# Optimization experiments

Measured on AMD Instinct MI355X. Metric: run time of the kernel, lower is better.

The kernel has to match this reference:

```python
import jax, jax.numpy as jnp
import numpy as np

B, S, H, M = 8, 128, 768, 128
EPS = 1e-12


def setup_inputs() -> dict:
    key = jax.random.key(0)
    ks = jax.random.split(key, 8)
    seq_hiddens = jax.random.normal(ks[0], (B, S, H), dtype=jnp.float32)
    gamma = jnp.ones((H,), jnp.float32)
    beta = jnp.zeros((H,), jnp.float32)
    # conditional LN dense weights (torch Linear weight: (out, in)); small init so math stays stable
    w_beta = jax.random.normal(ks[1], (H, H), dtype=jnp.float32) * 0.02
    w_gamma = jax.random.normal(ks[2], (H, H), dtype=jnp.float32) * 0.02
    w_ent = jax.random.normal(ks[3], (H, M), dtype=jnp.float32) * 0.02
    w_head = jax.random.normal(ks[4], (H, M), dtype=jnp.float32) * 0.02
    w_tail = jax.random.normal(ks[5], (H, M), dtype=jnp.float32) * 0.02
    b_ent = jnp.zeros((M,), jnp.float32)
    b_head = jnp.zeros((M,), jnp.float32)
    b_tail = jnp.zeros((M,), jnp.float32)
    return dict(seq_hiddens=seq_hiddens, gamma=gamma, beta=beta, w_beta=w_beta,
                w_gamma=w_gamma, w_ent=w_ent, b_ent=b_ent, w_head=w_head,
                b_head=b_head, w_tail=w_tail, b_tail=b_tail)


def _handshake_cln(seq, gamma, beta, w_beta, w_gamma):
    # Triangular pair expansion in the same row-major order as the torch loop:
    # for ind in range(S): pairs (ind, ind), (ind, ind+1), ..., (ind, S-1)
    s = seq.shape[1]
    ii, jj = jnp.triu_indices(s)                 # (P,) each, P = S(S+1)/2
    x = seq[:, jj, :]                            # visible hiddens   (B, P, H)
    cond = seq[:, ii, :]                         # repeated hiddens  (B, P, H)
    beta_c = jnp.einsum('bph,oh->bpo', cond, w_beta) + beta      # (B, P, H)
    gamma_c = jnp.einsum('bph,oh->bpo', cond, w_gamma) + gamma   # (B, P, H)
    mean = jnp.mean(x, axis=-1, keepdims=True)
    out = x - mean
    var = jnp.mean(out * out, axis=-1, keepdims=True)
    std = (var + EPS) ** 2                       # NOTE: faithful to source (no sqrt)
    return out / std * gamma_c + beta_c


def reference(seq_hiddens, gamma, beta, w_beta, w_gamma, w_ent, b_ent,
              w_head, b_head, w_tail, b_tail):
    shaking = _handshake_cln(seq_hiddens, gamma, beta, w_beta, w_gamma)  # (B, P, H)
    ent = jnp.tanh(shaking @ w_ent + b_ent)      # (B, P, M)
    head = jnp.tanh(shaking @ w_head + b_head)
    tail = jnp.tanh(shaking @ w_tail + b_tail)
    return jnp.stack([ent, head, tail], axis=0)  # (3, B, P, M)
```

## Files before the change

kernel.cpp:

```cpp
#include <hip/hip_runtime.h>
#include <hip/hip_bf16.h>
#include <hip/hip_fp16.h>
#include <math.h>

#define B_   8
#define S_   128
#define H_   768
#define M_   128
#define P_   8256
#define BP_  66048
#define EPSF 1e-12f

typedef unsigned short u16;
typedef unsigned int   u32;
typedef _Float16 h16;
typedef _Float16 ffrag __attribute__((ext_vector_type(8)));
typedef float    f32x16 __attribute__((ext_vector_type(16)));

__device__ __forceinline__ u32 fuse2(u32 x, u32 g, u32 b) {
    __half2 r = __hfma2(__builtin_bit_cast(__half2, x),
                        __builtin_bit_cast(__half2, g),
                        __builtin_bit_cast(__half2, b));
    return __builtin_bit_cast(u32, r);
}
__device__ __forceinline__ float fast_tanh(float v) {
    float t = __expf(v + v);
    float r = __builtin_amdgcn_rcpf(t + 1.0f);
    return fmaf(-2.0f, r, 1.0f);
}
__device__ __forceinline__ void gl_lds16(const h16* g, h16* l) {
    __builtin_amdgcn_global_load_lds(
        (const __attribute__((address_space(1))) u32*)g,
        (__attribute__((address_space(3))) u32*)l, 16, 0, 0);
}
__device__ __forceinline__ uint4 cvt8(float4 a, float4 b) {
    h16 v[8];
    v[0] = (h16)a.x; v[1] = (h16)a.y; v[2] = (h16)a.z; v[3] = (h16)a.w;
    v[4] = (h16)b.x; v[5] = (h16)b.y; v[6] = (h16)b.z; v[7] = (h16)b.w;
    return *reinterpret_cast<uint4*>(v);
}

#define CONDB 768
#define WPK0  768
#define BIAS0 792
#define NORM0 794
__global__ __launch_bounds__(256) void k_pre(
    const float* __restrict__ seq,
    const float* __restrict__ wg, const float* __restrict__ wb,
    const float* __restrict__ we, const float* __restrict__ wh,
    const float* __restrict__ wt,
    const float* __restrict__ gamma, const float* __restrict__ beta,
    const float* __restrict__ be, const float* __restrict__ bh,
    const float* __restrict__ bt,
    h16* __restrict__ wpk, float* __restrict__ biasc,
    h16* __restrict__ xn, h16* __restrict__ Gc, h16* __restrict__ Bc)
{
    __shared__ __align__(16) char smem[24576];
    const int bx = blockIdx.x;
    const int t = threadIdx.x;

    if (bx < CONDB) {
        h16* Ash = (h16*)smem;
        h16* Bsh = (h16*)smem + 64 * 72;
        const int rbx = bx & 15, by = bx >> 4;
        const int row0 = rbx * 64;
        const bool isg = (by < 24);
        const int nc0 = (isg ? by : by - 24) * 32;
        const float* wsrc = isg ? wg : wb;

        const int r = t >> 2, q = t & 3;
        const float* ap = seq + (size_t)(row0 + r) * H_ + q * 16;
        h16* asto = &Ash[r * 72 + q * 16];
        const int rb = t >> 3, qb = t & 7;
        const float* wp = wsrc + (size_t)(nc0 + rb) * H_ + qb * 8;
        h16* bsto = &Bsh[rb * 72 + qb * 8];

        const int lane = t & 63, wid = t >> 6;
        const int wm0 = (wid >> 1) * 32, wn0 = (wid & 1) * 16;
        const int l15 = lane & 15, quad = lane >> 4, q8 = quad * 8;

        typedef float f32x4 __attribute__((ext_vector_type(4)));
        f32x4 acc[2] = {};
        for (int kt = 0; kt < 12; ++kt) {
            const int k0 = kt * 64;
            float4 a0 = *(const float4*)(ap + k0);      float4 a1 = *(const float4*)(ap + k0 + 4);
            float4 a2 = *(const float4*)(ap + k0 + 8);  float4 a3 = *(const float4*)(ap + k0 + 12);
            float4 w0 = *(const float4*)(wp + k0);      float4 w1 = *(const float4*)(wp + k0 + 4);
            *(uint4*)asto = cvt8(a0, a1); *(uint4*)(asto + 8) = cvt8(a2, a3);
            *(uint4*)bsto = cvt8(w0, w1);
            __syncthreads();
#pragma unroll
            for (int ks = 0; ks < 64; ks += 32) {
                ffrag af[2], bf;
#pragma unroll
                for (int mi = 0; mi < 2; ++mi)
                    af[mi] = *reinterpret_cast<const ffrag*>(&Ash[(wm0 + mi * 16 + l15) * 72 + ks + q8]);
                bf = *reinterpret_cast<const ffrag*>(&Bsh[(wn0 + l15) * 72 + ks + q8]);
#pragma unroll
                for (int mi = 0; mi < 2; ++mi)
                    acc[mi] = __builtin_amdgcn_mfma_f32_16x16x32_f16(af[mi], bf, acc[mi], 0, 0, 0);
            }
            __syncthreads();
        }

        const float* bias = isg ? gamma : beta;
        h16* outp = isg ? Gc : Bc;
#pragma unroll
        for (int mi = 0; mi < 2; ++mi) {
            int c = wn0 + l15;
            float bv = bias[nc0 + c];
#pragma unroll
            for (int reg = 0; reg < 4; ++reg) {
                int rg = wm0 + mi * 16 + quad * 4 + reg;
                outp[(size_t)(row0 + rg) * H_ + nc0 + c] = (h16)(acc[mi][reg] + bv);
            }
        }
        return;
    }

    if (bx < BIAS0) {
        const int kt = bx - WPK0;
        float* stage = (float*)smem;
#pragma unroll
        for (int pass = 0; pass < 2; ++pass) {
            if (pass) __syncthreads();
            int f = t;
#pragma unroll
            for (int k = 0; k < 6; ++k, f += 256) {
                int head = f >> 9, rem = f & 511;
                int r = rem >> 5, m4 = rem & 31;
                const float* src = (head == 0) ? we : (head == 1 ? wh : wt);
                *(float4*)(stage + (size_t)(head * 16 + r) * 128 + m4 * 4) =
                    *(const float4*)(src + (size_t)(kt * 32 + pass * 16 + r) * 128 + m4 * 4);
            }
            __syncthreads();
#pragma unroll
            for (int e2 = 0; e2 < 3; ++e2) {
                int s = t + 256 * e2;
                int nbw = s >> 8, rem = s & 255;
                int chl = rem >> 7, nl = rem & 127;
                h16 v[8];
#pragma unroll
                for (int e = 0; e < 8; ++e)
                    v[e] = (h16)stage[(size_t)(nbw * 16 + chl * 8 + e) * 128 + nl];
                *(uint4*)(wpk + (size_t)nbw * 98304 + kt * 4096 +
                          ((pass * 2 + chl) * 128 + nl) * 8) = *(uint4*)v;
            }
            f = t;
        }
        return;
    }

    if (bx < NORM0) {
        int n = (bx - BIAS0) * 256 + t;
        if (n < 384)
            biasc[n] = (n < 128) ? be[n] : (n < 256 ? bh[n - 128] : bt[n - 256]);
        return;
    }

    float* red = (float*)smem;
    const int row = bx - NORM0;
    const int lane = t & 63, wid = t >> 6;
    const float* x = seq + (size_t)row * H_;
    float x0 = x[t], x1 = x[t + 256], x2 = x[t + 512];

    float s = x0 + x1 + x2;
    for (int o = 32; o; o >>= 1) s += __shfl_xor(s, o);
    if (lane == 0) red[wid] = s;
    __syncthreads();
    float mean = (red[0] + red[1] + red[2] + red[3]) * (1.0f / 768.0f);

    float c0 = x0 - mean, c1 = x1 - mean, c2 = x2 - mean;
    float ss = c0 * c0 + c1 * c1 + c2 * c2;
    for (int o = 32; o; o >>= 1) ss += __shfl_xor(ss, o);
    __syncthreads();
    if (lane == 0) red[wid] = ss;
    __syncthreads();
    float var = (red[0] + red[1] + red[2] + red[3]) * (1.0f / 768.0f);
    float sd = var + EPSF;
    float scale = 1.0f / (sd * sd);

    h16* xr = xn + (size_t)row * H_;
    xr[t] = (h16)(c0 * scale); xr[t + 256] = (h16)(c1 * scale); xr[t + 512] = (h16)(c2 * scale);
}

__global__ __launch_bounds__(256, 6) void k_pair_gemm(
    const h16* __restrict__ Xn, const h16* __restrict__ Gcb, const h16* __restrict__ Bcb,
    const h16* __restrict__ Wpk, const float* __restrict__ biasc,
    float* __restrict__ out)
{
    __shared__ h16 Ash[2][4 * 64 * 8];
    __shared__ h16 Bsh[2][4 * 128 * 8];

    const int t = threadIdx.x;
    const int nb = blockIdx.x;
    const int row0 = blockIdx.y * 64;

    const int r_s = t >> 2, c4 = t & 3;
    int gp = row0 + r_s;
    int b = gp / P_;
    int p = gp - b * P_;
    int i = (int)((257.0f - sqrtf(66049.0f - 8.0f * (float)p)) * 0.5f);
    if (i < 0) i = 0; if (i > 127) i = 127;
    while (i > 0 && (i * (257 - i)) / 2 > p) --i;
    while (((i + 1) * (256 - i)) / 2 <= p) ++i;
    int j = i + (p - (i * (257 - i)) / 2);

    const h16* xp  = Xn  + (size_t)(b * 128 + j) * H_ + c4 * 8;
    const h16* gp_ = Gcb + (size_t)(b * 128 + i) * H_ + c4 * 8;
    const h16* bp_ = Bcb + (size_t)(b * 128 + i) * H_ + c4 * 8;
    const int aw = (c4 * 64 + r_s) * 8;

    const h16* wtile = Wpk + (size_t)nb * 24 * 4096;
    const int wud = t & ~63;

    const int lane = t & 63, wid = t >> 6;
    const int wm0 = (wid >> 1) * 32, wn0 = (wid & 1) * 64;
    const int l31 = lane & 31, hi = lane >> 5;

#pragma unroll
    for (int c = 0; c < 2; ++c)
        gl_lds16(wtile + (size_t)(c * 256 + t) * 8, &Bsh[0][(c * 256 + wud) * 8]);
    {
        uint4 xa = *(const uint4*)xp;
        uint4 ga = *(const uint4*)gp_;
        uint4 ba = *(const uint4*)bp_;
        uint4 f;
        f.x = fuse2(xa.x, ga.x, ba.x); f.y = fuse2(xa.y, ga.y, ba.y);
        f.z = fuse2(xa.z, ga.z, ba.z); f.w = fuse2(xa.w, ga.w, ba.w);
        *(uint4*)&Ash[0][aw] = f;
    }
    __syncthreads();

    f32x16 acc[2] = {};
#pragma unroll 2
    for (int kt = 0; kt < 24; ++kt) {
        const int buf = kt & 1, nbf = buf ^ 1;
        uint4 xa, ga, ba;
        if (kt < 23) {
            const h16* wnext = wtile + (size_t)(kt + 1) * 4096;
#pragma unroll
            for (int c = 0; c < 2; ++c)
                gl_lds16(wnext + (size_t)(c * 256 + t) * 8, &Bsh[nbf][(c * 256 + wud) * 8]);
            const int k0 = (kt + 1) * 32;
            xa = *(const uint4*)(xp + k0);
            ga = *(const uint4*)(gp_ + k0);
            ba = *(const uint4*)(bp_ + k0);
        }

#pragma unroll
        for (int ks = 0; ks < 2; ++ks) {
            const int ch0 = ks * 2;
            ffrag af, bf[2];
            af = *reinterpret_cast<const ffrag*>(
                &Ash[buf][((ch0 + hi) * 64 + wm0 + l31) * 8]);
#pragma unroll
            for (int ni = 0; ni < 2; ++ni)
                bf[ni] = *reinterpret_cast<const ffrag*>(
                    &Bsh[buf][((ch0 + hi) * 128 + wn0 + ni * 32 + l31) * 8]);
#pragma unroll
            for (int ni = 0; ni < 2; ++ni)
                acc[ni] = __builtin_amdgcn_mfma_f32_32x32x16_f16(af, bf[ni], acc[ni], 0, 0, 0);
        }

        if (kt < 23) {
            uint4 f;
            f.x = fuse2(xa.x, ga.x, ba.x); f.y = fuse2(xa.y, ga.y, ba.y);
            f.z = fuse2(xa.z, ga.z, ba.z); f.w = fuse2(xa.w, ga.w, ba.w);
            *(uint4*)&Ash[nbf][aw] = f;
        }
        __syncthreads();
    }

#pragma unroll
    for (int ni = 0; ni < 2; ++ni) {
        int c = wn0 + ni * 32 + l31;
        float bv = biasc[nb * 128 + c];
#pragma unroll
        for (int reg = 0; reg < 16; ++reg) {
            int rg = wm0 + (reg & 3) + 8 * (reg >> 2) + 4 * hi;
            __builtin_nontemporal_store(fast_tanh(acc[ni][reg] + bv),
                &out[((size_t)nb * BP_ + row0 + rg) * M_ + c]);
        }
    }
}

extern "C" void kernel_launch(void* const* d_in, const int* in_sizes, int n_in,
                              void* d_out, int out_size, void* d_ws, size_t ws_size,
                              hipStream_t stream)
{
    const float* seq     = (const float*)d_in[0];
    const float* gamma   = (const float*)d_in[1];
    const float* beta    = (const float*)d_in[2];
    const float* w_beta  = (const float*)d_in[3];
    const float* w_gamma = (const float*)d_in[4];
    const float* w_ent   = (const float*)d_in[5];
    const float* b_ent   = (const float*)d_in[6];
    const float* w_head  = (const float*)d_in[7];
    const float* b_head  = (const float*)d_in[8];
    const float* w_tail  = (const float*)d_in[9];
    const float* b_tail  = (const float*)d_in[10];
    float* out = (float*)d_out;

    char* ws = (char*)d_ws;
    h16* xn    = (h16*)ws; ws += (size_t)1024 * 768 * 2;
    h16* wpk   = (h16*)ws; ws += (size_t)294912 * 2;
    h16* gc    = (h16*)ws; ws += (size_t)1024 * 768 * 2;
    h16* bc    = (h16*)ws; ws += (size_t)1024 * 768 * 2;
    float* biasc = (float*)ws; ws += 384 * 4;

    hipLaunchKernelGGL(k_pre, dim3(NORM0 + 1024), dim3(256), 0, stream,
                       seq, w_gamma, w_beta, w_ent, w_head, w_tail,
                       gamma, beta, b_ent, b_head, b_tail,
                       wpk, biasc, xn, gc, bc);
    hipLaunchKernelGGL(k_pair_gemm, dim3(3, 1032), dim3(256), 0, stream,
                       xn, gc, bc, wpk, biasc, out);
}
```

Baseline: 202.3 us.

## Enlarge pair-GEMM tile to 128x128 with K=64 stages and swizzled LDS

The pair GEMM block tile grows from 64 to 128 rows and the K step from 32 to 64, so each wave computes a 2x2 grid of 32x32 MFMA tiles. This halves the grid and increases reuse of each loaded weight and activation fragment. The A tile in LDS gets an XOR swizzle to avoid bank conflicts. Global loads are interleaved across sub-steps with explicit barriers and raised wave priority around the MFMAs. The cost is more LDS and registers per block, with occupancy capped at 2 blocks per SM, which leaves less latency hiding from other waves.

```diff
diff --git a/kernel.cpp b/kernel.cpp
--- a/kernel.cpp
+++ b/kernel.cpp
@@ -146,7 +146,6 @@
                 *(uint4*)(wpk + (size_t)nbw * 98304 + kt * 4096 +
                           ((pass * 2 + chl) * 128 + nl) * 8) = *(uint4*)v;
             }
-            f = t;
         }
         return;
     }
@@ -184,19 +183,19 @@
     xr[t] = (h16)(c0 * scale); xr[t + 256] = (h16)(c1 * scale); xr[t + 512] = (h16)(c2 * scale);
 }
 
-__global__ __launch_bounds__(256, 6) void k_pair_gemm(
+__global__ __launch_bounds__(256, 2) void k_pair_gemm(
     const h16* __restrict__ Xn, const h16* __restrict__ Gcb, const h16* __restrict__ Bcb,
     const h16* __restrict__ Wpk, const float* __restrict__ biasc,
     float* __restrict__ out)
 {
-    __shared__ h16 Ash[2][4 * 64 * 8];
-    __shared__ h16 Bsh[2][4 * 128 * 8];
+    __shared__ h16 Ash[2][8 * 128 * 8];
+    __shared__ h16 Bsh[2][8 * 128 * 8];
 
     const int t = threadIdx.x;
     const int nb = blockIdx.x;
-    const int row0 = blockIdx.y * 64;
-
-    const int r_s = t >> 2, c4 = t & 3;
+    const int row0 = blockIdx.y * 128;
+
+    const int r_s = t >> 1, c2 = t & 1;
     int gp = row0 + r_s;
     int b = gp / P_;
     int p = gp - b * P_;
@@ -206,83 +205,118 @@
     while (((i + 1) * (256 - i)) / 2 <= p) ++i;
     int j = i + (p - (i * (257 - i)) / 2);
 
-    const h16* xp  = Xn  + (size_t)(b * 128 + j) * H_ + c4 * 8;
-    const h16* gp_ = Gcb + (size_t)(b * 128 + i) * H_ + c4 * 8;
-    const h16* bp_ = Bcb + (size_t)(b * 128 + i) * H_ + c4 * 8;
-    const int aw = (c4 * 64 + r_s) * 8;
-
-    const h16* wtile = Wpk + (size_t)nb * 24 * 4096;
+    const h16* xp  = Xn  + (size_t)(b * 128 + j) * H_ + c2 * 32;
+    const h16* gp_ = Gcb + (size_t)(b * 128 + i) * H_ + c2 * 32;
+    const h16* bp_ = Bcb + (size_t)(b * 128 + i) * H_ + c2 * 32;
+    int aw[4];
+#pragma unroll
+    for (int u = 0; u < 4; ++u) {
+        int ch = 4 * c2 + u;
+        aw[u] = ((ch * 128 + r_s) ^ (ch << 1)) * 8;
+    }
+
+    const h16* wtile = Wpk + (size_t)nb * 98304;
     const int wud = t & ~63;
 
     const int lane = t & 63, wid = t >> 6;
-    const int wm0 = (wid >> 1) * 32, wn0 = (wid & 1) * 64;
+    const int wm0 = (wid >> 1) * 64, wn0 = (wid & 1) * 64;
     const int l31 = lane & 31, hi = lane >> 5;
 
-#pragma unroll
-    for (int c = 0; c < 2; ++c)
-        gl_lds16(wtile + (size_t)(c * 256 + t) * 8, &Bsh[0][(c * 256 + wud) * 8]);
     {
-        uint4 xa = *(const uint4*)xp;
-        uint4 ga = *(const uint4*)gp_;
-        uint4 ba = *(const uint4*)bp_;
-        uint4 f;
-        f.x = fuse2(xa.x, ga.x, ba.x); f.y = fuse2(xa.y, ga.y, ba.y);
-        f.z = fuse2(xa.z, ga.z, ba.z); f.w = fuse2(xa.w, ga.w, ba.w);
-        *(uint4*)&Ash[0][aw] = f;
-    }
-    __syncthreads();
-
-    f32x16 acc[2] = {};
-#pragma unroll 2
-    for (int kt = 0; kt < 24; ++kt) {
+        uint4 xa[4], ga[4], ba[4];
+#pragma unroll
+        for (int u = 0; u < 4; ++u) {
+            xa[u] = *(const uint4*)(xp + u * 8);
+            ga[u] = *(const uint4*)(gp_ + u * 8);
+            ba[u] = *(const uint4*)(bp_ + u * 8);
+        }
+#pragma unroll
+        for (int u = 0; u < 4; ++u) {
+            uint4 f;
+            f.x = fuse2(xa[u].x, ga[u].x, ba[u].x); f.y = fuse2(xa[u].y, ga[u].y, ba[u].y);
+            f.z = fuse2(xa[u].z, ga[u].z, ba[u].z); f.w = fuse2(xa[u].w, ga[u].w, ba[u].w);
+            *(uint4*)&Ash[0][aw[u]] = f;
+        }
+#pragma unroll
+        for (int s = 0; s < 4; ++s)
+            gl_lds16(wtile + (size_t)(s * 256 + t) * 8, &Bsh[0][(s * 256 + wud) * 8]);
+    }
+    asm volatile("s_waitcnt vmcnt(0) lgkmcnt(0)" ::: "memory");
+    __builtin_amdgcn_s_barrier();
+
+    f32x16 acc[2][2] = {};
+    for (int kt = 0; kt < 12; ++kt) {
         const int buf = kt & 1, nbf = buf ^ 1;
-        uint4 xa, ga, ba;
-        if (kt < 23) {
-            const h16* wnext = wtile + (size_t)(kt + 1) * 4096;
-#pragma unroll
-            for (int c = 0; c < 2; ++c)
-                gl_lds16(wnext + (size_t)(c * 256 + t) * 8, &Bsh[nbf][(c * 256 + wud) * 8]);
-            const int k0 = (kt + 1) * 32;
-            xa = *(const uint4*)(xp + k0);
-            ga = *(const uint4*)(gp_ + k0);
-            ba = *(const uint4*)(bp_ + k0);
-        }
-
-#pragma unroll
-        for (int ks = 0; ks < 2; ++ks) {
-            const int ch0 = ks * 2;
-            ffrag af, bf[2];
-            af = *reinterpret_cast<const ffrag*>(
-                &Ash[buf][((ch0 + hi) * 64 + wm0 + l31) * 8]);
+        const h16* wnext = wtile + (size_t)(kt + 1) * 8192;
+        const int k0 = (kt + 1) * 64;
+        uint4 xa[4], ga[4], ba[4];
+#pragma unroll
+        for (int s = 0; s < 4; ++s) {
+            if (kt < 11) {
+                if (s == 0) {
+                    gl_lds16(wnext + (size_t)(0 * 256 + t) * 8, &Bsh[nbf][(0 * 256 + wud) * 8]);
+                    gl_lds16(wnext + (size_t)(1 * 256 + t) * 8, &Bsh[nbf][(1 * 256 + wud) * 8]);
+                } else if (s == 1) {
+                    gl_lds16(wnext + (size_t)(2 * 256 + t) * 8, &Bsh[nbf][(2 * 256 + wud) * 8]);
+                    gl_lds16(wnext + (size_t)(3 * 256 + t) * 8, &Bsh[nbf][(3 * 256 + wud) * 8]);
+                } else if (s == 2) {
+#pragma unroll
+                    for (int u = 0; u < 4; ++u) {
+                        xa[u] = *(const uint4*)(xp + k0 + u * 8);
+                        ga[u] = *(const uint4*)(gp_ + k0 + u * 8);
+                        ba[u] = *(const uint4*)(bp_ + k0 + u * 8);
+                    }
+                }
+            }
+            const int ch = 2 * s + hi;
+            ffrag af[2], bf[2];
+#pragma unroll
+            for (int mi = 0; mi < 2; ++mi)
+                af[mi] = *reinterpret_cast<const ffrag*>(
+                    &Ash[buf][((ch * 128 + wm0 + mi * 32 + l31) ^ (ch << 1)) * 8]);
 #pragma unroll
             for (int ni = 0; ni < 2; ++ni)
                 bf[ni] = *reinterpret_cast<const ffrag*>(
-                    &Bsh[buf][((ch0 + hi) * 128 + wn0 + ni * 32 + l31) * 8]);
-#pragma unroll
-            for (int ni = 0; ni < 2; ++ni)
-                acc[ni] = __builtin_amdgcn_mfma_f32_32x32x16_f16(af, bf[ni], acc[ni], 0, 0, 0);
-        }
-
-        if (kt < 23) {
-            uint4 f;
-            f.x = fuse2(xa.x, ga.x, ba.x); f.y = fuse2(xa.y, ga.y, ba.y);
-            f.z = fuse2(xa.z, ga.z, ba.z); f.w = fuse2(xa.w, ga.w, ba.w);
-            *(uint4*)&Ash[nbf][aw] = f;
-        }
-        __syncthreads();
-    }
-
-#pragma unroll
-    for (int ni = 0; ni < 2; ++ni) {
-        int c = wn0 + ni * 32 + l31;
-        float bv = biasc[nb * 128 + c];
-#pragma unroll
-        for (int reg = 0; reg < 16; ++reg) {
-            int rg = wm0 + (reg & 3) + 8 * (reg >> 2) + 4 * hi;
-            __builtin_nontemporal_store(fast_tanh(acc[ni][reg] + bv),
-                &out[((size_t)nb * BP_ + row0 + rg) * M_ + c]);
-        }
-    }
+                    &Bsh[buf][(ch * 128 + wn0 + ni * 32 + l31) * 8]);
+            __builtin_amdgcn_sched_barrier(0);
+            __builtin_amdgcn_s_barrier();
+            __builtin_amdgcn_s_setprio(1);
+#pragma unroll
+            for (int mi = 0; mi < 2; ++mi)
+#pragma unroll
+                for (int ni = 0; ni < 2; ++ni)
+                    acc[mi][ni] = __builtin_amdgcn_mfma_f32_32x32x16_f16(af[mi], bf[ni], acc[mi][ni], 0, 0, 0);
+            __builtin_amdgcn_s_setprio(0);
+            if (s == 3) {
+                if (kt < 11) {
+#pragma unroll
+                    for (int u = 0; u < 4; ++u) {
+                        uint4 f;
+                        f.x = fuse2(xa[u].x, ga[u].x, ba[u].x); f.y = fuse2(xa[u].y, ga[u].y, ba[u].y);
+                        f.z = fuse2(xa[u].z, ga[u].z, ba[u].z); f.w = fuse2(xa[u].w, ga[u].w, ba[u].w);
+                        *(uint4*)&Ash[nbf][aw[u]] = f;
+                    }
+                }
+                asm volatile("s_waitcnt lgkmcnt(0)" ::: "memory");
+                __builtin_amdgcn_sched_barrier(0);
+            }
+            __builtin_amdgcn_s_barrier();
+        }
+    }
+
+#pragma unroll
+    for (int mi = 0; mi < 2; ++mi)
+#pragma unroll
+        for (int ni = 0; ni < 2; ++ni) {
+            int c = wn0 + ni * 32 + l31;
+            float bv = biasc[nb * 128 + c];
+#pragma unroll
+            for (int reg = 0; reg < 16; ++reg) {
+                int rg = wm0 + mi * 32 + (reg & 3) + 8 * (reg >> 2) + 4 * hi;
+                __builtin_nontemporal_store(fast_tanh(acc[mi][ni][reg] + bv),
+                    &out[((size_t)nb * BP_ + row0 + rg) * M_ + c]);
+            }
+        }
 }
 
 extern "C" void kernel_launch(void* const* d_in, const int* in_sizes, int n_in,
@@ -313,6 +347,6 @@
                        seq, w_gamma, w_beta, w_ent, w_head, w_tail,
                        gamma, beta, b_ent, b_head, b_tail,
                        wpk, biasc, xn, gc, bc);
-    hipLaunchKernelGGL(k_pair_gemm, dim3(3, 1032), dim3(256), 0, stream,
+    hipLaunchKernelGGL(k_pair_gemm, dim3(3, 516), dim3(256), 0, stream,
                        xn, gc, bc, wpk, biasc, out);
 }
```

Result: slower. 222.6 us (+10.1%).
